# Performance work log

Hardware: AMD Instinct MI355X
Metric: run time of the kernel (lower is better)

Reference implementation:

```python
import jax, jax.numpy as jnp
import numpy as np

V, E, H0, H1 = 32000, 512, 1024, 1024
B, S = 32, 128


def setup_inputs() -> dict:
    key = jax.random.key(0)
    ks = jax.random.split(key, 10)
    s = 0.02
    tokens = jax.random.randint(ks[0], (B, S), 0, V)
    emb = jax.random.normal(ks[1], (V, E), dtype=jnp.float32) * s
    W0 = jax.random.normal(ks[2], (E, H0), dtype=jnp.float32) * s
    U0 = jax.random.normal(ks[3], (H0, H0), dtype=jnp.float32) * s
    b0 = jnp.zeros((H0,), dtype=jnp.float32)
    W1 = jax.random.normal(ks[4], (H0, H1), dtype=jnp.float32) * s
    U1 = jax.random.normal(ks[5], (H1, H1), dtype=jnp.float32) * s
    b1 = jnp.zeros((H1,), dtype=jnp.float32)
    Wd = jax.random.normal(ks[6], (H1, V), dtype=jnp.float32) * s
    bd = jnp.zeros((V,), dtype=jnp.float32)
    return {"tokens": tokens, "emb": emb, "W0": W0, "U0": U0, "b0": b0,
            "W1": W1, "U1": U1, "b1": b1, "Wd": Wd, "bd": bd}


def reference(tokens, emb, W0, U0, b0, W1, U1, b1, Wd, bd):
    # Embedding lookup: [B, S, E]
    x = emb[tokens]
    # Stacked SimpleRNN: h_t = tanh(x W + h U + b), layer1 feeds layer2 per step.
    xt = jnp.swapaxes(x, 0, 1)  # [S, B, E] for scan over time

    def step(carry, x_t):
        h0, h1 = carry
        h0 = jnp.tanh(x_t @ W0 + h0 @ U0 + b0)
        h1 = jnp.tanh(h0 @ W1 + h1 @ U1 + b1)
        return (h0, h1), h1

    batch = tokens.shape[0]
    init = (jnp.zeros((batch, W0.shape[1]), dtype=x.dtype),
            jnp.zeros((batch, W1.shape[1]), dtype=x.dtype))
    _, ys = jax.lax.scan(step, init, xt)  # ys: [S, B, H1]
    ys = jnp.swapaxes(ys, 0, 1)  # [B, S, H1]
    # Final dense to vocab logits: [B, S, V]
    return ys @ Wd + bd
```

## Files before the change

kernel.cpp:

```cpp
#include <hip/hip_runtime.h>
#include <hip/hip_bf16.h>
#include <cstdint>

typedef __attribute__((ext_vector_type(8))) short bf16x8;
typedef __attribute__((ext_vector_type(4))) float f32x4;
typedef __attribute__((ext_vector_type(4))) unsigned int u32x4;

#define V_ 32000
#define E_ 512
#define H_ 1024
#define B_ 32
#define S_ 128

#define L1WG 16
#define L2WG 32
#define NWGS 48

typedef __attribute__((address_space(1))) unsigned int* gas1_t;
typedef __attribute__((address_space(3))) unsigned int* las3_t;
__device__ __forceinline__ void load_lds16(const void* g, void* l) {
  __builtin_amdgcn_global_load_lds((gas1_t)g, (las3_t)l, 16, 0, 0);
}

__device__ __forceinline__ void ldx4_sc(u32x4* d, const void* p) {
  asm volatile("global_load_dwordx4 %0, %1, off sc0 sc1" : "=v"(*d) : "v"(p) : "memory");
}
__device__ __forceinline__ unsigned ld_sc(const unsigned* p) {
  unsigned d;
  asm volatile("global_load_dword %0, %1, off sc0 sc1\n\ts_waitcnt vmcnt(0)"
               : "=v"(d) : "v"(p) : "memory");
  return d;
}
__device__ __forceinline__ void st_swap(unsigned* p, unsigned v) {
  asm volatile("global_atomic_swap %0, %1, off sc1" :: "v"(p), "v"(v) : "memory");
}
__device__ __forceinline__ void st_swap2(uint2* p, uint2 v) {
  asm volatile("global_atomic_swap_x2 %0, %1, off sc1" :: "v"(p), "v"(v) : "memory");
}
#define WAITVM0()                                     \
  asm volatile("s_waitcnt vmcnt(0)" ::: "memory");    \
  __builtin_amdgcn_sched_barrier(0)

__device__ __forceinline__ unsigned short bfbits(float x) {
  __hip_bfloat16 b = __float2bfloat16(x);
  union { __hip_bfloat16 b; unsigned short u; } c;
  c.b = b;
  return c.u;
}

__device__ __forceinline__ uint2 pack_rows(const float f[4], int lane, int j) {
  uint2 v2[4];
#pragma unroll
  for (int r = 0; r < 4; ++r) {
    const float o = __shfl_xor(f[r], 1);
    const float lo = (lane & 1) ? o : f[r];
    const float hi = (lane & 1) ? f[r] : o;
    const unsigned pk = (unsigned)bfbits(lo) | ((unsigned)bfbits(hi) << 16);
    const unsigned q2 = __shfl_xor(pk, 2);
    v2[r].x = (j & 2) ? q2 : pk;
    v2[r].y = (j & 2) ? pk : q2;
  }
  const int rs = lane & 3;
  return rs == 0 ? v2[0] : rs == 1 ? v2[1] : rs == 2 ? v2[2] : v2[3];
}

__global__ __launch_bounds__(256) void transpose_f32_bf16(
    const float* __restrict__ src, __hip_bfloat16* __restrict__ dst, int R, int C) {
  __shared__ float tile[32][33];
  const int c0 = blockIdx.x << 5, r0 = blockIdx.y << 5;
  const int tx = threadIdx.x & 31, ty = threadIdx.x >> 5;
#pragma unroll
  for (int i = 0; i < 32; i += 8)
    tile[ty + i][tx] = src[(size_t)(r0 + ty + i) * C + (c0 + tx)];
  __syncthreads();
#pragma unroll
  for (int i = 0; i < 32; i += 8)
    dst[(size_t)(c0 + ty + i) * R + (r0 + tx)] = __float2bfloat16(tile[tx][ty + i]);
}

__global__ __launch_bounds__(256) void gather_embed(
    const int* __restrict__ tokens, const float* __restrict__ emb,
    __hip_bfloat16* __restrict__ Xg) {
  const int r = blockIdx.x;
  const int t = r >> 5, b = r & 31;
  const int tok = tokens[b * S_ + t];
  const float* e = emb + (size_t)tok * E_;
  __hip_bfloat16* o = Xg + (size_t)r * E_;
  for (int k = threadIdx.x; k < E_; k += 256) o[k] = __float2bfloat16(e[k]);
}

__global__ __launch_bounds__(256) void make_frag_w(
    const float* __restrict__ W, __hip_bfloat16* __restrict__ F) {
  const int idx = blockIdx.x * 256 + threadIdx.x;
  const int lane = idx & 63, kb = (idx >> 6) & 31, g = idx >> 11;
  const int j = (g << 4) + (lane & 15);
  const int kbase = (kb << 5) + ((lane >> 4) << 3);
  __hip_bfloat16* o = F + (size_t)idx * 8;
#pragma unroll
  for (int e = 0; e < 8; ++e) o[e] = __float2bfloat16(W[(size_t)(kbase + e) * H_ + j]);
}

__global__ __launch_bounds__(256) void gemm_bf16_tn(
    const __hip_bfloat16* __restrict__ A, const __hip_bfloat16* __restrict__ Bt,
    const float* __restrict__ bias, float* __restrict__ C, int M, int N, int K) {
  __shared__ __hip_bfloat16 ldsA[2][128 * 64];
  __shared__ __hip_bfloat16 ldsB[2][128 * 64];
  const int nwg = gridDim.x * gridDim.y;
  int L = blockIdx.y * gridDim.x + blockIdx.x;
  L = ((L & 7) * (nwg >> 3)) + (L >> 3);
  const int m0 = (L / gridDim.x) << 7;
  const int n0 = (L % gridDim.x) << 7;
  const int tid = threadIdx.x, wave = tid >> 6, lane = tid & 63;
  const int wr = wave >> 1, wc = wave & 1;
  f32x4 acc[4][4];
#pragma unroll
  for (int i = 0; i < 4; ++i)
#pragma unroll
    for (int jj = 0; jj < 4; ++jj) acc[i][jj] = (f32x4){0.f, 0.f, 0.f, 0.f};

  auto stage = [&](int buf, int k0) {
#pragma unroll
    for (int i = 0; i < 4; ++i) {
      const int c = i * 4 + wave;
      const int idx = (c << 6) + lane;
      const int row = idx >> 3, kk = (idx & 7) << 3;
      load_lds16(A + (size_t)(m0 + row) * K + (k0 + kk), &ldsA[buf][c * 512]);
      load_lds16(Bt + (size_t)(n0 + row) * K + (k0 + kk), &ldsB[buf][c * 512]);
    }
  };

  stage(0, 0);
  __syncthreads();
  int cur = 0;
  for (int k0 = 0; k0 < K; k0 += 64) {
    if (k0 + 64 < K) stage(cur ^ 1, k0 + 64);
    __builtin_amdgcn_s_setprio(1);
#pragma unroll
    for (int ks = 0; ks < 2; ++ks) {
      bf16x8 af[4], bfr[4];
#pragma unroll
      for (int mi = 0; mi < 4; ++mi)
        af[mi] = *(const bf16x8*)(&ldsA[cur][0] +
                                  (((wr << 6) + (mi << 4) + (lane & 15)) << 6) +
                                  (ks << 5) + ((lane >> 4) << 3));
#pragma unroll
      for (int ni = 0; ni < 4; ++ni)
        bfr[ni] = *(const bf16x8*)(&ldsB[cur][0] +
                                   (((wc << 6) + (ni << 4) + (lane & 15)) << 6) +
                                   (ks << 5) + ((lane >> 4) << 3));
#pragma unroll
      for (int mi = 0; mi < 4; ++mi)
#pragma unroll
        for (int ni = 0; ni < 4; ++ni)
          acc[mi][ni] =
              __builtin_amdgcn_mfma_f32_16x16x32_bf16(af[mi], bfr[ni], acc[mi][ni], 0, 0, 0);
    }
    __builtin_amdgcn_s_setprio(0);
    __syncthreads();
    cur ^= 1;
  }
#pragma unroll
  for (int mi = 0; mi < 4; ++mi) {
#pragma unroll
    for (int ni = 0; ni < 4; ++ni) {
      const int n = n0 + (wc << 6) + (ni << 4) + (lane & 15);
      const float bn = bias[n];
#pragma unroll
      for (int r = 0; r < 4; ++r) {
        const int m = m0 + (wr << 6) + (mi << 4) + ((lane >> 4) << 2) + r;
        C[(size_t)m * N + n] = acc[mi][ni][r] + bn;
      }
    }
  }
}

__global__ __launch_bounds__(512, 2) void rnn_recur(
    const __hip_bfloat16* __restrict__ U0f, const __hip_bfloat16* __restrict__ W1f,
    const __hip_bfloat16* __restrict__ U1f, const float* __restrict__ xw,
    const float* __restrict__ b1,
    __hip_bfloat16* __restrict__ h0buf,
    __hip_bfloat16* __restrict__ h1buf,
    __hip_bfloat16* __restrict__ Y,
    unsigned* __restrict__ flags) {
  __shared__ char smem[135168];
  char* sA0 = smem;
  char* sA1 = smem + 65536;
  float* pad = (float*)(smem + 131072);

  const int g = blockIdx.x;
  const bool isL1 = (g < L1WG);
  const int tid = threadIdx.x, wave = tid >> 6, lane = tid & 63;
  const int mi = wave & 1;
  const int cg = isL1 ? (wave >> 1) : ((wave >> 1) & 1);
  const int mat = isL1 ? 0 : (wave >> 2);
  const int colbase = isL1 ? (g << 6) : ((g - L1WG) << 5);
  const int j = colbase + (cg << 4) + (lane & 15);
  const int gg = (colbase >> 4) + cg;
  const int rowbase = (mi << 4) + ((lane >> 4) << 2);
  const int rs = lane & 3;
  const int ra = (mi << 4) + (lane & 15);
  const int q4 = (lane >> 4) << 4;
  const float b1j = b1[j];

  const __hip_bfloat16* wb = isL1 ? U0f : (mat == 0 ? W1f : U1f);
  bf16x8 wfr[32];
#pragma unroll
  for (int kb = 0; kb < 32; ++kb)
    wfr[kb] = *(const bf16x8*)(wb + (size_t)((((gg << 5) + kb) << 6) + lane) * 8);

  if (!isL1) {
    for (int i = tid; i < 4096; i += 512) *(uint4*)(sA1 + i * 16) = (uint4){0u, 0u, 0u, 0u};
  }
  __syncthreads();

  const int stg_row = tid >> 7;
  const int stg_colb = (tid & 127) << 4;
  const unsigned* fpoll = flags + ((lane < NWGS ? lane : NWGS - 1) << 4);

  if (isL1) {
    for (int p = 0; p < S_; ++p) {
      const float* xrow = xw + ((size_t)p << 15);
      float xv[4];
#pragma unroll
      for (int r = 0; r < 4; ++r) xv[r] = xrow[(rowbase + r) * H_ + j];
      if (p >= 1) {
        const unsigned tgt =
            (lane < L1WG) ? (unsigned)p : (p >= 3 ? (unsigned)(p - 3) : 0u);
        unsigned v;
        do { v = ld_sc(fpoll); } while (__any(v < tgt));
        const char* src0 = (const char*)(h0buf + ((size_t)((p - 1) & 3) << 15));
        u32x4 t0[8];
#pragma unroll
        for (int i = 0; i < 8; ++i) ldx4_sc(&t0[i], src0 + (size_t)(((i << 9) + tid) << 4));
        WAITVM0();
#pragma unroll
        for (int i = 0; i < 8; ++i) {
          const int row = stg_row + (i << 2);
          *(u32x4*)(sA0 + (row << 11) + (stg_colb ^ ((row & 7) << 4))) = t0[i];
        }
        __syncthreads();
      }
      f32x4 acc = {0.f, 0.f, 0.f, 0.f};
      if (p >= 1) {
#pragma unroll
        for (int kb = 0; kb < 32; ++kb) {
          bf16x8 a = *(const bf16x8*)(
              sA0 + (ra << 11) + ((((kb << 6) + q4)) ^ ((ra & 7) << 4)));
          acc = __builtin_amdgcn_mfma_f32_16x16x32_bf16(a, wfr[kb], acc, 0, 0, 0);
        }
      }
      float f[4];
#pragma unroll
      for (int r = 0; r < 4; ++r) f[r] = tanhf(acc[r] + xv[r]);
      uint2 vsel = pack_rows(f, lane, j);
      uint2* h4 = (uint2*)(h0buf + ((size_t)(p & 3) << 15));
      st_swap2(h4 + (rowbase + rs) * (H_ / 4) + (j >> 2), vsel);
      WAITVM0();
      __syncthreads();
      if (tid == 0) st_swap(flags + (g << 4), (unsigned)(p + 1));
    }
  } else {
    for (int t = 0; t < S_; ++t) {
      {
        const unsigned tgt = (lane < L1WG) ? (unsigned)(t + 1) : (unsigned)t;
        unsigned v;
        do { v = ld_sc(fpoll); } while (__any(v < tgt));
      }
      {
        const char* src0 = (const char*)(h0buf + ((size_t)(t & 3) << 15));
        u32x4 t0[8], t1[8];
#pragma unroll
        for (int i = 0; i < 8; ++i) ldx4_sc(&t0[i], src0 + (size_t)(((i << 9) + tid) << 4));
        if (t >= 1) {
          const char* src1 = (const char*)(h1buf + ((size_t)((t - 1) & 1) << 15));
#pragma unroll
          for (int i = 0; i < 8; ++i) ldx4_sc(&t1[i], src1 + (size_t)(((i << 9) + tid) << 4));
        }
        WAITVM0();
#pragma unroll
        for (int i = 0; i < 8; ++i) {
          const int row = stg_row + (i << 2);
          *(u32x4*)(sA0 + (row << 11) + (stg_colb ^ ((row & 7) << 4))) = t0[i];
        }
        if (t >= 1) {
#pragma unroll
          for (int i = 0; i < 8; ++i) {
            const int row = stg_row + (i << 2);
            *(u32x4*)(sA1 + (row << 11) + (stg_colb ^ ((row & 7) << 4))) = t1[i];
          }
        }
        __syncthreads();
      }
      const char* sA = (mat == 0) ? sA0 : sA1;
      f32x4 acc = {0.f, 0.f, 0.f, 0.f};
#pragma unroll
      for (int kb = 0; kb < 32; ++kb) {
        bf16x8 a = *(const bf16x8*)(
            sA + (ra << 11) + ((((kb << 6) + q4)) ^ ((ra & 7) << 4)));
        acc = __builtin_amdgcn_mfma_f32_16x16x32_bf16(a, wfr[kb], acc, 0, 0, 0);
      }
      const int pair = wave & 3;
      if (mat == 0) *(f32x4*)(pad + pair * 256 + lane * 4) = acc;
      __syncthreads();
      if (mat == 1) {
        f32x4 accW = *(const f32x4*)(pad + pair * 256 + lane * 4);
        float f[4];
#pragma unroll
        for (int r = 0; r < 4; ++r) f[r] = tanhf(acc[r] + accW[r] + b1j);
        uint2 vsel = pack_rows(f, lane, j);
        const int bb = rowbase + rs;
        ((uint2*)Y)[((size_t)bb * S_ + t) * (H_ / 4) + (j >> 2)] = vsel;
        uint2* h4 = (uint2*)(h1buf + ((size_t)(t & 1) << 15));
        st_swap2(h4 + bb * (H_ / 4) + (j >> 2), vsel);
      }
      WAITVM0();
      __syncthreads();
      if (tid == 0) st_swap(flags + (g << 4), (unsigned)(t + 1));
    }
  }
}

extern "C" void kernel_launch(void* const* d_in, const int* in_sizes, int n_in, void* d_out,
                              int out_size, void* d_ws, size_t ws_size, hipStream_t stream) {
  const int* tokens = (const int*)d_in[0];
  const float* emb = (const float*)d_in[1];
  const float* W0 = (const float*)d_in[2];
  const float* U0 = (const float*)d_in[3];
  const float* b0 = (const float*)d_in[4];
  const float* W1 = (const float*)d_in[5];
  const float* U1 = (const float*)d_in[6];
  const float* b1 = (const float*)d_in[7];
  const float* Wd = (const float*)d_in[8];
  const float* bd = (const float*)d_in[9];
  float* out = (float*)d_out;

  char* ws = (char*)d_ws;
  __hip_bfloat16* Wdt = (__hip_bfloat16*)ws;  ws += (size_t)V_ * H_ * 2;
  __hip_bfloat16* W0t = (__hip_bfloat16*)ws;  ws += (size_t)H_ * E_ * 2;
  __hip_bfloat16* Xg = (__hip_bfloat16*)ws;   ws += (size_t)4096 * E_ * 2;
  __hip_bfloat16* U0f = (__hip_bfloat16*)ws;  ws += (size_t)H_ * H_ * 2;
  __hip_bfloat16* W1f = (__hip_bfloat16*)ws;  ws += (size_t)H_ * H_ * 2;
  __hip_bfloat16* U1f = (__hip_bfloat16*)ws;  ws += (size_t)H_ * H_ * 2;
  float* xw = (float*)ws;                     ws += (size_t)4096 * H_ * 4;
  __hip_bfloat16* h0buf = (__hip_bfloat16*)ws; ws += 4 * B_ * H_ * 2;
  __hip_bfloat16* h1buf = (__hip_bfloat16*)ws; ws += 2 * B_ * H_ * 2;
  __hip_bfloat16* Y = (__hip_bfloat16*)ws;    ws += (size_t)4096 * H_ * 2;
  unsigned* flags = (unsigned*)ws;            ws += 4096;

  transpose_f32_bf16<<<dim3(V_ / 32, H_ / 32), 256, 0, stream>>>(Wd, Wdt, H_, V_);
  transpose_f32_bf16<<<dim3(H_ / 32, E_ / 32), 256, 0, stream>>>(W0, W0t, E_, H_);
  gather_embed<<<4096, 256, 0, stream>>>(tokens, emb, Xg);
  make_frag_w<<<512, 256, 0, stream>>>(U0, U0f);
  make_frag_w<<<512, 256, 0, stream>>>(W1, W1f);
  make_frag_w<<<512, 256, 0, stream>>>(U1, U1f);
  hipMemsetAsync(flags, 0, 4096, stream);

  gemm_bf16_tn<<<dim3(H_ / 128, 4096 / 128), 256, 0, stream>>>(Xg, W0t, b0, xw, 4096, H_, E_);

  rnn_recur<<<NWGS, 512, 0, stream>>>(U0f, W1f, U1f, xw, b1, h0buf, h1buf, Y, flags);

  gemm_bf16_tn<<<dim3(V_ / 128, 4096 / 128), 256, 0, stream>>>(Y, Wdt, bd, out, 4096, V_, H_);
}
```

Baseline: 1.259 ms.

## Fuse vocab projection GEMM into recurrence kernel with flag-gated streaming tiles

Merges the RNN recurrence and the final vocab GEMM into one launch. Extra workgroups each wait on the layer-2 progress flags for their 8 timesteps, then compute a 256x128 logits tile. Y is now stored time-major so a tile covers complete finished timesteps, and the output row index is remapped on store. The aim is to overlap the large vocab GEMM with the serial recurrence instead of running it afterwards. The risks are deadlock or contention if GEMM blocks take the CUs the 48 recurrence blocks need, launch bounds dropping to one block per CU, and coherent (sc) global loads for A replacing async LDS loads.

```diff
diff --git a/kernel.cpp b/kernel.cpp
--- a/kernel.cpp
+++ b/kernel.cpp
@@ -15,6 +15,8 @@
 #define L1WG 16
 #define L2WG 32
 #define NWGS 48
+#define NTILES 250
+#define GWGS (16 * NTILES)
 
 typedef __attribute__((address_space(1))) unsigned int* gas1_t;
 typedef __attribute__((address_space(3))) unsigned int* las3_t;
@@ -128,7 +130,6 @@
       load_lds16(Bt + (size_t)(n0 + row) * K + (k0 + kk), &ldsB[buf][c * 512]);
     }
   };
-
   stage(0, 0);
   __syncthreads();
   int cur = 0;
@@ -174,148 +175,259 @@
   }
 }
 
-__global__ __launch_bounds__(512, 2) void rnn_recur(
+__global__ __launch_bounds__(512, 1) void rnn_vocab_fused(
     const __hip_bfloat16* __restrict__ U0f, const __hip_bfloat16* __restrict__ W1f,
     const __hip_bfloat16* __restrict__ U1f, const float* __restrict__ xw,
     const float* __restrict__ b1,
     __hip_bfloat16* __restrict__ h0buf,
     __hip_bfloat16* __restrict__ h1buf,
     __hip_bfloat16* __restrict__ Y,
-    unsigned* __restrict__ flags) {
+    unsigned* __restrict__ flags,
+    const __hip_bfloat16* __restrict__ Wdt,
+    const float* __restrict__ bd, float* __restrict__ out) {
   __shared__ char smem[135168];
-  char* sA0 = smem;
-  char* sA1 = smem + 65536;
-  float* pad = (float*)(smem + 131072);
-
-  const int g = blockIdx.x;
-  const bool isL1 = (g < L1WG);
   const int tid = threadIdx.x, wave = tid >> 6, lane = tid & 63;
-  const int mi = wave & 1;
-  const int cg = isL1 ? (wave >> 1) : ((wave >> 1) & 1);
-  const int mat = isL1 ? 0 : (wave >> 2);
-  const int colbase = isL1 ? (g << 6) : ((g - L1WG) << 5);
-  const int j = colbase + (cg << 4) + (lane & 15);
-  const int gg = (colbase >> 4) + cg;
-  const int rowbase = (mi << 4) + ((lane >> 4) << 2);
-  const int rs = lane & 3;
-  const int ra = (mi << 4) + (lane & 15);
-  const int q4 = (lane >> 4) << 4;
-  const float b1j = b1[j];
-
-  const __hip_bfloat16* wb = isL1 ? U0f : (mat == 0 ? W1f : U1f);
-  bf16x8 wfr[32];
-#pragma unroll
-  for (int kb = 0; kb < 32; ++kb)
-    wfr[kb] = *(const bf16x8*)(wb + (size_t)((((gg << 5) + kb) << 6) + lane) * 8);
-
-  if (!isL1) {
-    for (int i = tid; i < 4096; i += 512) *(uint4*)(sA1 + i * 16) = (uint4){0u, 0u, 0u, 0u};
-  }
-  __syncthreads();
-
-  const int stg_row = tid >> 7;
-  const int stg_colb = (tid & 127) << 4;
-  const unsigned* fpoll = flags + ((lane < NWGS ? lane : NWGS - 1) << 4);
-
-  if (isL1) {
-    for (int p = 0; p < S_; ++p) {
-      const float* xrow = xw + ((size_t)p << 15);
-      float xv[4];
-#pragma unroll
-      for (int r = 0; r < 4; ++r) xv[r] = xrow[(rowbase + r) * H_ + j];
-      if (p >= 1) {
-        const unsigned tgt =
-            (lane < L1WG) ? (unsigned)p : (p >= 3 ? (unsigned)(p - 3) : 0u);
-        unsigned v;
-        do { v = ld_sc(fpoll); } while (__any(v < tgt));
-        const char* src0 = (const char*)(h0buf + ((size_t)((p - 1) & 3) << 15));
-        u32x4 t0[8];
-#pragma unroll
-        for (int i = 0; i < 8; ++i) ldx4_sc(&t0[i], src0 + (size_t)(((i << 9) + tid) << 4));
+
+  if (blockIdx.x < NWGS) {
+    char* sA0 = smem;
+    char* sA1 = smem + 65536;
+    float* pad = (float*)(smem + 131072);
+    const int g = blockIdx.x;
+    const bool isL1 = (g < L1WG);
+    const int mi = wave & 1;
+    const int cg = isL1 ? (wave >> 1) : ((wave >> 1) & 1);
+    const int mat = isL1 ? 0 : (wave >> 2);
+    const int colbase = isL1 ? (g << 6) : ((g - L1WG) << 5);
+    const int j = colbase + (cg << 4) + (lane & 15);
+    const int gg = (colbase >> 4) + cg;
+    const int rowbase = (mi << 4) + ((lane >> 4) << 2);
+    const int rs = lane & 3;
+    const int ra = (mi << 4) + (lane & 15);
+    const int q4 = (lane >> 4) << 4;
+    const float b1j = b1[j];
+
+    const __hip_bfloat16* wb = isL1 ? U0f : (mat == 0 ? W1f : U1f);
+    bf16x8 wfr[32];
+#pragma unroll
+    for (int kb = 0; kb < 32; ++kb)
+      wfr[kb] = *(const bf16x8*)(wb + (size_t)((((gg << 5) + kb) << 6) + lane) * 8);
+
+    if (!isL1) {
+      for (int i = tid; i < 4096; i += 512) *(uint4*)(sA1 + i * 16) = (uint4){0u, 0u, 0u, 0u};
+    }
+    __syncthreads();
+
+    const int stg_row = tid >> 7;
+    const int stg_colb = (tid & 127) << 4;
+    const unsigned* fpoll = flags + ((lane < NWGS ? lane : NWGS - 1) << 4);
+
+    if (isL1) {
+      for (int p = 0; p < S_; ++p) {
+        const float* xrow = xw + ((size_t)p << 15);
+        float xv[4];
+#pragma unroll
+        for (int r = 0; r < 4; ++r) xv[r] = xrow[(rowbase + r) * H_ + j];
+        if (p >= 1) {
+          const unsigned tgt =
+              (lane < L1WG) ? (unsigned)p : (p >= 3 ? (unsigned)(p - 3) : 0u);
+          unsigned v;
+          do { v = ld_sc(fpoll); } while (__any(v < tgt));
+          const char* src0 = (const char*)(h0buf + ((size_t)((p - 1) & 3) << 15));
+          u32x4 t0[8];
+#pragma unroll
+          for (int i = 0; i < 8; ++i) ldx4_sc(&t0[i], src0 + (size_t)(((i << 9) + tid) << 4));
+          WAITVM0();
+#pragma unroll
+          for (int i = 0; i < 8; ++i) {
+            const int row = stg_row + (i << 2);
+            *(u32x4*)(sA0 + (row << 11) + (stg_colb ^ ((row & 7) << 4))) = t0[i];
+          }
+          __syncthreads();
+        }
+        f32x4 acc = {0.f, 0.f, 0.f, 0.f};
+        if (p >= 1) {
+#pragma unroll
+          for (int kb = 0; kb < 32; ++kb) {
+            bf16x8 a = *(const bf16x8*)(
+                sA0 + (ra << 11) + ((((kb << 6) + q4)) ^ ((ra & 7) << 4)));
+            acc = __builtin_amdgcn_mfma_f32_16x16x32_bf16(a, wfr[kb], acc, 0, 0, 0);
+          }
+        }
+        float f[4];
+#pragma unroll
+        for (int r = 0; r < 4; ++r) f[r] = tanhf(acc[r] + xv[r]);
+        uint2 vsel = pack_rows(f, lane, j);
+        uint2* h4 = (uint2*)(h0buf + ((size_t)(p & 3) << 15));
+        st_swap2(h4 + (rowbase + rs) * (H_ / 4) + (j >> 2), vsel);
         WAITVM0();
-#pragma unroll
-        for (int i = 0; i < 8; ++i) {
-          const int row = stg_row + (i << 2);
-          *(u32x4*)(sA0 + (row << 11) + (stg_colb ^ ((row & 7) << 4))) = t0[i];
-        }
         __syncthreads();
+        if (tid == 0) st_swap(flags + (g << 4), (unsigned)(p + 1));
       }
-      f32x4 acc = {0.f, 0.f, 0.f, 0.f};
-      if (p >= 1) {
+    } else {
+      for (int t = 0; t < S_; ++t) {
+        {
+          const unsigned tgt = (lane < L1WG) ? (unsigned)(t + 1) : (unsigned)t;
+          unsigned v;
+          do { v = ld_sc(fpoll); } while (__any(v < tgt));
+        }
+        {
+          const char* src0 = (const char*)(h0buf + ((size_t)(t & 3) << 15));
+          u32x4 t0[8], t1[8];
+#pragma unroll
+          for (int i = 0; i < 8; ++i) ldx4_sc(&t0[i], src0 + (size_t)(((i << 9) + tid) << 4));
+          if (t >= 1) {
+            const char* src1 = (const char*)(h1buf + ((size_t)((t - 1) & 1) << 15));
+#pragma unroll
+            for (int i = 0; i < 8; ++i) ldx4_sc(&t1[i], src1 + (size_t)(((i << 9) + tid) << 4));
+          }
+          WAITVM0();
+#pragma unroll
+          for (int i = 0; i < 8; ++i) {
+            const int row = stg_row + (i << 2);
+            *(u32x4*)(sA0 + (row << 11) + (stg_colb ^ ((row & 7) << 4))) = t0[i];
+          }
+          if (t >= 1) {
+#pragma unroll
+            for (int i = 0; i < 8; ++i) {
+              const int row = stg_row + (i << 2);
+              *(u32x4*)(sA1 + (row << 11) + (stg_colb ^ ((row & 7) << 4))) = t1[i];
+            }
+          }
+          __syncthreads();
+        }
+        const char* sA = (mat == 0) ? sA0 : sA1;
+        f32x4 acc = {0.f, 0.f, 0.f, 0.f};
 #pragma unroll
         for (int kb = 0; kb < 32; ++kb) {
           bf16x8 a = *(const bf16x8*)(
-              sA0 + (ra << 11) + ((((kb << 6) + q4)) ^ ((ra & 7) << 4)));
+              sA + (ra << 11) + ((((kb << 6) + q4)) ^ ((ra & 7) << 4)));
           acc = __builtin_amdgcn_mfma_f32_16x16x32_bf16(a, wfr[kb], acc, 0, 0, 0);
         }
+        const int pair = wave & 3;
+        if (mat == 0) *(f32x4*)(pad + pair * 256 + lane * 4) = acc;
+        __syncthreads();
+        if (mat == 1) {
+          f32x4 accW = *(const f32x4*)(pad + pair * 256 + lane * 4);
+          float f[4];
+#pragma unroll
+          for (int r = 0; r < 4; ++r) f[r] = tanhf(acc[r] + accW[r] + b1j);
+          uint2 vsel = pack_rows(f, lane, j);
+          const int bb = rowbase + rs;
+          uint2* h4 = (uint2*)(h1buf + ((size_t)(t & 1) << 15));
+          st_swap2(h4 + bb * (H_ / 4) + (j >> 2), vsel);
+          st_swap2((uint2*)Y + ((size_t)((t << 5) + bb)) * (H_ / 4) + (j >> 2), vsel);
+        }
+        WAITVM0();
+        __syncthreads();
+        if (tid == 0) st_swap(flags + (g << 4), (unsigned)(t + 1));
       }
-      float f[4];
-#pragma unroll
-      for (int r = 0; r < 4; ++r) f[r] = tanhf(acc[r] + xv[r]);
-      uint2 vsel = pack_rows(f, lane, j);
-      uint2* h4 = (uint2*)(h0buf + ((size_t)(p & 3) << 15));
-      st_swap2(h4 + (rowbase + rs) * (H_ / 4) + (j >> 2), vsel);
+    }
+    return;
+  }
+
+  const int bid = blockIdx.x - NWGS;
+  const int mt = bid / NTILES, nt = bid - mt * NTILES;
+  const int m0 = mt << 8, n0 = nt << 7;
+  {
+    const unsigned tgt = (unsigned)((mt << 3) + 8);
+    if (wave == 0) {
+      const unsigned* fp = flags + ((L1WG + (lane & 31)) << 4);
+      while (true) {
+        unsigned v = ld_sc(fp);
+        if (!__any(v < tgt)) break;
+        asm volatile("s_sleep 8");
+      }
+    }
+    __syncthreads();
+  }
+  __hip_bfloat16* ldsA = (__hip_bfloat16*)smem;
+  __hip_bfloat16* ldsB = (__hip_bfloat16*)(smem + 65536);
+  const int wr = wave >> 1, wc = wave & 1;
+  f32x4 acc[4][4];
+#pragma unroll
+  for (int i = 0; i < 4; ++i)
+#pragma unroll
+    for (int jj = 0; jj < 4; ++jj) acc[i][jj] = (f32x4){0.f, 0.f, 0.f, 0.f};
+
+  u32x4 ta[4];
+  auto issueA = [&](int k0) {
+#pragma unroll
+    for (int i = 0; i < 4; ++i) {
+      const int chunk = (i << 9) + tid;
+      const int row = chunk >> 3, kk = (chunk & 7) << 3;
+      ldx4_sc(&ta[i], Y + (size_t)(m0 + row) * H_ + k0 + kk);
+    }
+  };
+  auto issueB = [&](int buf, int k0) {
+#pragma unroll
+    for (int i = 0; i < 2; ++i) {
+      const int c = (i << 3) + wave;
+      const int idx = (c << 6) + lane;
+      const int row = idx >> 3, kk = (idx & 7) << 3;
+      load_lds16(Wdt + (size_t)(n0 + row) * H_ + k0 + kk, ldsB + buf * 8192 + c * 512);
+    }
+  };
+  auto writeA = [&](int buf) {
+#pragma unroll
+    for (int i = 0; i < 4; ++i) {
+      const int chunk = (i << 9) + tid;
+      *(u32x4*)((char*)ldsA + buf * 32768 + chunk * 16) = ta[i];
+    }
+  };
+
+  issueA(0);
+  issueB(0, 0);
+  WAITVM0();
+  writeA(0);
+  __syncthreads();
+  int cur = 0;
+  for (int k0 = 0; k0 < H_; k0 += 64) {
+    const bool more = (k0 + 64 < H_);
+    if (more) {
+      issueA(k0 + 64);
+      issueB(cur ^ 1, k0 + 64);
+    }
+    __builtin_amdgcn_s_setprio(1);
+#pragma unroll
+    for (int ks = 0; ks < 2; ++ks) {
+      bf16x8 af[4], bfr[4];
+#pragma unroll
+      for (int mi = 0; mi < 4; ++mi)
+        af[mi] = *(const bf16x8*)(ldsA + cur * 16384 +
+                                  (((wr << 6) + (mi << 4) + (lane & 15)) << 6) +
+                                  (ks << 5) + ((lane >> 4) << 3));
+#pragma unroll
+      for (int ni = 0; ni < 4; ++ni)
+        bfr[ni] = *(const bf16x8*)(ldsB + cur * 8192 +
+                                   (((ni << 4) + (lane & 15)) << 6) +
+                                   (ks << 5) + ((lane >> 4) << 3) + (wc << 12));
+#pragma unroll
+      for (int mi = 0; mi < 4; ++mi)
+#pragma unroll
+        for (int ni = 0; ni < 4; ++ni)
+          acc[mi][ni] =
+              __builtin_amdgcn_mfma_f32_16x16x32_bf16(af[mi], bfr[ni], acc[mi][ni], 0, 0, 0);
+    }
+    __builtin_amdgcn_s_setprio(0);
+    if (more) {
       WAITVM0();
-      __syncthreads();
-      if (tid == 0) st_swap(flags + (g << 4), (unsigned)(p + 1));
-    }
-  } else {
-    for (int t = 0; t < S_; ++t) {
-      {
-        const unsigned tgt = (lane < L1WG) ? (unsigned)(t + 1) : (unsigned)t;
-        unsigned v;
-        do { v = ld_sc(fpoll); } while (__any(v < tgt));
+      writeA(cur ^ 1);
+    }
+    __syncthreads();
+    cur ^= 1;
+  }
+#pragma unroll
+  for (int mi = 0; mi < 4; ++mi) {
+#pragma unroll
+    for (int ni = 0; ni < 4; ++ni) {
+      const int n = n0 + (wc << 6) + (ni << 4) + (lane & 15);
+      const float bn = bd[n];
+#pragma unroll
+      for (int r = 0; r < 4; ++r) {
+        const int m = m0 + (wr << 6) + (mi << 4) + ((lane >> 4) << 2) + r;
+        const size_t orow = (size_t)(m & 31) * S_ + (m >> 5);
+        out[orow * V_ + n] = acc[mi][ni][r] + bn;
       }
-      {
-        const char* src0 = (const char*)(h0buf + ((size_t)(t & 3) << 15));
-        u32x4 t0[8], t1[8];
-#pragma unroll
-        for (int i = 0; i < 8; ++i) ldx4_sc(&t0[i], src0 + (size_t)(((i << 9) + tid) << 4));
-        if (t >= 1) {
-          const char* src1 = (const char*)(h1buf + ((size_t)((t - 1) & 1) << 15));
-#pragma unroll
-          for (int i = 0; i < 8; ++i) ldx4_sc(&t1[i], src1 + (size_t)(((i << 9) + tid) << 4));
-        }
-        WAITVM0();
-#pragma unroll
-        for (int i = 0; i < 8; ++i) {
-          const int row = stg_row + (i << 2);
-          *(u32x4*)(sA0 + (row << 11) + (stg_colb ^ ((row & 7) << 4))) = t0[i];
-        }
-        if (t >= 1) {
-#pragma unroll
-          for (int i = 0; i < 8; ++i) {
-            const int row = stg_row + (i << 2);
-            *(u32x4*)(sA1 + (row << 11) + (stg_colb ^ ((row & 7) << 4))) = t1[i];
-          }
-        }
-        __syncthreads();
-      }
-      const char* sA = (mat == 0) ? sA0 : sA1;
-      f32x4 acc = {0.f, 0.f, 0.f, 0.f};
-#pragma unroll
-      for (int kb = 0; kb < 32; ++kb) {
-        bf16x8 a = *(const bf16x8*)(
-            sA + (ra << 11) + ((((kb << 6) + q4)) ^ ((ra & 7) << 4)));
-        acc = __builtin_amdgcn_mfma_f32_16x16x32_bf16(a, wfr[kb], acc, 0, 0, 0);
-      }
-      const int pair = wave & 3;
-      if (mat == 0) *(f32x4*)(pad + pair * 256 + lane * 4) = acc;
-      __syncthreads();
-      if (mat == 1) {
-        f32x4 accW = *(const f32x4*)(pad + pair * 256 + lane * 4);
-        float f[4];
-#pragma unroll
-        for (int r = 0; r < 4; ++r) f[r] = tanhf(acc[r] + accW[r] + b1j);
-        uint2 vsel = pack_rows(f, lane, j);
-        const int bb = rowbase + rs;
-        ((uint2*)Y)[((size_t)bb * S_ + t) * (H_ / 4) + (j >> 2)] = vsel;
-        uint2* h4 = (uint2*)(h1buf + ((size_t)(t & 1) << 15));
-        st_swap2(h4 + bb * (H_ / 4) + (j >> 2), vsel);
-      }
-      WAITVM0();
-      __syncthreads();
-      if (tid == 0) st_swap(flags + (g << 4), (unsigned)(t + 1));
     }
   }
 }
@@ -357,7 +469,6 @@
 
   gemm_bf16_tn<<<dim3(H_ / 128, 4096 / 128), 256, 0, stream>>>(Xg, W0t, b0, xw, 4096, H_, E_);
 
-  rnn_recur<<<NWGS, 512, 0, stream>>>(U0f, W1f, U1f, xw, b1, h0buf, h1buf, Y, flags);
-
-  gemm_bf16_tn<<<dim3(V_ / 128, 4096 / 128), 256, 0, stream>>>(Y, Wdt, bd, out, 4096, V_, H_);
-}
+  rnn_vocab_fused<<<NWGS + GWGS, 512, 0, stream>>>(U0f, W1f, U1f, xw, b1, h0buf, h1buf, Y,
+                                                   flags, Wdt, bd, out);
+}
```

Result: faster. 1.077 ms (-14.5%).
